# Kernel optimization log

Measured on AMD Instinct MI355X. Metric: run time of the kernel, lower is better.

## Reference

```python
import jax, jax.numpy as jnp
import numpy as np

PH = 12        # planning_horizon
B = 16         # batch
H = 256        # belief dim
Z = 64         # state dim
CAND = 512     # candidates
TOPK = 64      # top_candidates
ITERS = 3      # optimisation_iters
NTOOLS = 36    # num_tools
CONT = 2       # cont_action_size (hard-coded in source)
MIN_A, MAX_A = -1.0, 1.0


def setup_inputs() -> dict:
    ks = jax.random.split(jax.random.key(0), 9)
    s = 0.05  # weight scale keeps tanh in its linear-ish regime
    return {
        "belief": jax.random.normal(ks[0], (B, H), jnp.float32),
        "state": jax.random.normal(ks[1], (B, Z), jnp.float32),
        "Wb": jax.random.normal(ks[2], (H, H), jnp.float32) * s,
        "Wa": jax.random.normal(ks[3], (3, H), jnp.float32) * s,
        "bb": jnp.zeros((H,), jnp.float32),
        "Ws": jax.random.normal(ks[4], (H, Z), jnp.float32) * s,
        "bs": jnp.zeros((Z,), jnp.float32),
        "wrb": jax.random.normal(ks[5], (H,), jnp.float32) * s,
        "wrs": jax.random.normal(ks[6], (Z,), jnp.float32) * s,
    }


def reference(belief, state, Wb, Wa, bb, Ws, bs, wrb, wrs):
    # expand to (B*CAND, .) exactly like unsqueeze+expand+reshape (row-repeat)
    b0 = jnp.repeat(belief, CAND, axis=0)  # (B*CAND, H)
    s0 = jnp.repeat(state, CAND, axis=0)   # (B*CAND, Z)

    action_mean = jnp.zeros((PH, B, 1, CONT), jnp.float32)
    action_std = jnp.ones((PH, B, 1, CONT), jnp.float32)
    freq = jnp.ones((PH, B, 1, NTOOLS), jnp.float32)

    key = jax.random.key(42)
    for it in range(ITERS):
        k_disc, k_noise, key = jax.random.split(key, 3)
        # multinomial(freq, CAND, replacement=True) per (PH*B) row
        logits = jnp.log(freq.reshape(-1, NTOOLS))            # (PH*B, NTOOLS)
        disc = jax.random.categorical(k_disc, logits, shape=(CAND, PH * B)).T
        disc = disc.reshape(PH, B * CAND, 1).astype(jnp.float32)
        # continuous: mean + std * N(0,1), clamped
        noise = jax.random.normal(k_noise, (PH, B, CAND, CONT), jnp.float32)
        cont = jnp.clip(action_mean + action_std * noise, MIN_A, MAX_A)
        cont = cont.reshape(PH, B * CAND, CONT)
        actions = jnp.concatenate([disc, cont], axis=-1)       # (PH, B*CAND, 3)

        # rollout: stand-in recurrent transition + linear reward
        def step(carry, a_t):
            b, s_ = carry
            b = jnp.tanh(b @ Wb + a_t @ Wa + bb)
            s_ = jnp.tanh(b @ Ws + bs)
            return (b, s_), (b, s_)

        _, (beliefs, states) = jax.lax.scan(step, (b0, s0), actions)
        returns = (beliefs @ wrb + states @ wrs).sum(axis=0)   # (B*CAND,)

        # top-k candidates per batch element
        _, idx = jax.lax.top_k(returns.reshape(B, CAND), TOPK)  # (B, TOPK)
        actions_r = actions.reshape(PH, B, CAND, 1 + CONT)
        best = jnp.take_along_axis(actions_r, idx[None, :, :, None], axis=2)  # (PH,B,TOPK,3)

        cont_best = best[..., 1:]
        action_mean = cont_best.mean(axis=2, keepdims=True)
        action_std = jnp.std(cont_best, axis=2, keepdims=True)  # unbiased=False

        # batched histogram over TOPK discrete actions (histc with unit bins),
        # +1 smoothing, normalize -- one fused pass instead of PH*B histc calls
        dints = best[..., 0].astype(jnp.int32)                  # (PH, B, TOPK)
        hist = jax.nn.one_hot(dints, NTOOLS, dtype=jnp.float32).sum(axis=2) + 1.0
        freq = (hist / hist.sum(axis=-1, keepdims=True))[:, :, None, :]

    disc_final = jnp.argmax(freq[0, :, 0, :], axis=-1).astype(jnp.float32)[:, None]  # (B,1)
    cont_final = action_mean[0, :, 0, :]                                             # (B,CONT)
    return jnp.concatenate([disc_final, cont_final], axis=1)                         # (B,3)
```

## Files before the change

kernel.cpp:

```cpp
#include <hip/hip_runtime.h>
#include <cstdint>
#include <cmath>

#define PARTITIONABLE 1

constexpr int kPH = 12;
constexpr int kB = 16;
constexpr int kH = 256;
constexpr int kZ = 64;
constexpr int kCand = 512;
constexpr int kTopK = 64;
constexpr int kTools = 36;
constexpr int kRT = kB * kCand;
constexpr uint32_t kDiscTotal = (uint32_t)kCand * kPH * kB * kTools;
constexpr uint32_t kContTotal = (uint32_t)kPH * kB * kCand * 2;

constexpr int kRowsB = 16;
constexpr int kStrideB = 20;

__host__ __device__ inline void tf2x32(uint32_t k0, uint32_t k1,
                                       uint32_t x0, uint32_t x1,
                                       uint32_t& o0, uint32_t& o1) {
  uint32_t ks2 = k0 ^ k1 ^ 0x1BD11BDAu;
  x0 += k0; x1 += k1;
#define TFROT(v, d) (((v) << (d)) | ((v) >> (32 - (d))))
#define TFR(r) { x0 += x1; x1 = TFROT(x1, r); x1 ^= x0; }
  TFR(13) TFR(15) TFR(26) TFR(6)
  x0 += k1;  x1 += ks2 + 1u;
  TFR(17) TFR(29) TFR(16) TFR(24)
  x0 += ks2; x1 += k0 + 2u;
  TFR(13) TFR(15) TFR(26) TFR(6)
  x0 += k0;  x1 += k1 + 3u;
  TFR(17) TFR(29) TFR(16) TFR(24)
  x0 += k1;  x1 += ks2 + 4u;
  TFR(13) TFR(15) TFR(26) TFR(6)
  x0 += ks2; x1 += k0 + 5u;
#undef TFR
#undef TFROT
  o0 = x0; o1 = x1;
}

__device__ inline uint32_t jax_bits32(uint32_t k0, uint32_t k1,
                                      uint32_t idx, uint32_t total) {
#if PARTITIONABLE
  (void)total;
  uint32_t y0, y1;
  tf2x32(k0, k1, 0u, idx, y0, y1);
  return y0 ^ y1;
#else
  uint32_t half = total >> 1;
  uint32_t y0, y1;
  if (idx < half) { tf2x32(k0, k1, idx, idx + half, y0, y1); return y0; }
  else            { tf2x32(k0, k1, idx - half, idx, y0, y1); return y1; }
#endif
}

static void host_split3(uint32_t k0, uint32_t k1, uint32_t out[3][2]) {
#if PARTITIONABLE
  for (uint32_t i = 0; i < 3; ++i)
    tf2x32(k0, k1, 0u, i, out[i][0], out[i][1]);
#else
  uint32_t a0,a1,b0,b1,c0,c1;
  tf2x32(k0, k1, 0u, 3u, a0, a1);
  tf2x32(k0, k1, 1u, 4u, b0, b1);
  tf2x32(k0, k1, 2u, 5u, c0, c1);
  out[0][0]=a0; out[0][1]=b0;
  out[1][0]=c0; out[1][1]=a1;
  out[2][0]=b1; out[2][1]=c1;
#endif
}

__device__ inline float erfinv_xla(float x) {
  float xx = x * x;
  float w = -(float)log1p((double)(-xx));
  float p;
  if (w < 5.0f) {
    float ww = w - 2.5f;
    p = 2.81022636e-08f;
    p = fmaf(p, ww, 3.43273939e-07f);
    p = fmaf(p, ww, -3.5233877e-06f);
    p = fmaf(p, ww, -4.39150654e-06f);
    p = fmaf(p, ww, 0.00021858087f);
    p = fmaf(p, ww, -0.00125372503f);
    p = fmaf(p, ww, -0.00417768164f);
    p = fmaf(p, ww, 0.246640727f);
    p = fmaf(p, ww, 1.50140941f);
  } else {
    float ww = sqrtf(w) - 3.0f;
    p = -0.000200214257f;
    p = fmaf(p, ww, 0.000100950558f);
    p = fmaf(p, ww, 0.00134934322f);
    p = fmaf(p, ww, -0.00367342844f);
    p = fmaf(p, ww, 0.00573950773f);
    p = fmaf(p, ww, -0.0076224613f);
    p = fmaf(p, ww, 0.00943887047f);
    p = fmaf(p, ww, 1.00167406f);
    p = fmaf(p, ww, 2.83297682f);
  }
  return p * x;
}

__global__ __launch_bounds__(256) void k_sample_disc(
    uint32_t kd0, uint32_t kd1, const float* __restrict__ lfreq,
    float* __restrict__ discA, int it0) {
  int gid = blockIdx.x * 256 + threadIdx.x;
  if (gid >= kCand * kPH * kB) return;
  int c = gid / (kPH * kB);
  int j = gid - c * (kPH * kB);
  int best = 0;
  if (it0) {
    uint32_t bm = 0u;
    for (int t = 0; t < kTools; ++t) {
      uint32_t bits = jax_bits32(kd0, kd1, (uint32_t)(gid * kTools + t), kDiscTotal);
      uint32_t m = bits >> 9;
      if (t == 0 || m > bm) { bm = m; best = t; }
    }
  } else {
    const float* lf = lfreq + j * kTools;
    float bv = 0.0f;
    for (int t = 0; t < kTools; ++t) {
      uint32_t bits = jax_bits32(kd0, kd1, (uint32_t)(gid * kTools + t), kDiscTotal);
      float u = __uint_as_float((bits >> 9) | 0x3F800000u) - 1.0f;
      if (u == 0.0f) u = 1.17549435e-38f;
      float l1 = (float)log((double)u);
      float g = -(float)log((double)(-l1));
      float val = g + lf[t];
      if (t == 0 || val > bv) { bv = val; best = t; }
    }
  }
  int ph = j >> 4, b = j & 15;
  discA[ph * kRT + b * kCand + c] = (float)best;
}

__global__ __launch_bounds__(256) void k_sample_cont(
    uint32_t kn0, uint32_t kn1, const float* __restrict__ meanv,
    const float* __restrict__ stdv, float* __restrict__ contA, int it0) {
  int gid = blockIdx.x * 256 + threadIdx.x;
  if (gid >= (int)kContTotal) return;
  uint32_t bits = jax_bits32(kn0, kn1, (uint32_t)gid, kContTotal);
  float f = __uint_as_float((bits >> 9) | 0x3F800000u) - 1.0f;
  const float lo = -0.99999994f;
  float u = fmaxf(lo, f * 2.0f + lo);
  float n = __uint_as_float(0x3FB504F3u) * erfinv_xla(u);
  int d = gid & 1;
  int c = (gid >> 1) & (kCand - 1);
  int rest = gid >> 10;
  int ph = rest >> 4, b = rest & 15;
  float m, s;
  if (it0) { m = 0.0f; s = 1.0f; }
  else {
    m = meanv[rest * 2 + d];
    s = stdv[rest * 2 + d];
  }
  float x = m + s * n;
  x = fminf(fmaxf(x, -1.0f), 1.0f);
  contA[(ph * kRT + b * kCand + c) * 2 + d] = x;
}

__global__ __launch_bounds__(512, 4) void k_rollout(
    const float* __restrict__ belief,
    const float* __restrict__ discA, const float* __restrict__ contA,
    const float* __restrict__ Wb, const float* __restrict__ Wa,
    const float* __restrict__ bbv_, const float* __restrict__ Ws,
    const float* __restrict__ bs_, const float* __restrict__ wrb,
    const float* __restrict__ wrs, float* __restrict__ ret) {
  __shared__ float sBc[kH * kStrideB];
  __shared__ float pT[kRowsB * kH];
  __shared__ float sAD[kRowsB], sA0[kRowsB], sA1[kRowsB];
  __shared__ float sret[kRowsB];

  const int tid = threadIdx.x;
  const int row0 = blockIdx.x * kRowsB;
  const int batch = row0 >> 9;

  const int w = tid >> 6;
  const int kw = w >> 2;
  const int wc = w & 3;
  const int lane = tid & 63;
  const int lr = lane >> 5;
  const int lc = lane & 31;
  const int r0 = lr * 8;
  const int c0 = wc * 64 + lc * 2;
  const int kbase = kw * 128;

  const int lr2 = lane >> 4;
  const int lc2 = lane & 15;
  const int r0s = lr2 * 4;
  const int cs = wc * 16 + lc2;

  const float wa00 = Wa[c0],          wa01 = Wa[c0 + 1];
  const float wa10 = Wa[kH + c0],     wa11 = Wa[kH + c0 + 1];
  const float wa20 = Wa[2 * kH + c0], wa21 = Wa[2 * kH + c0 + 1];
  const float bb0 = bbv_[c0], bb1 = bbv_[c0 + 1];
  const float wrb0 = wrb[c0], wrb1 = wrb[c0 + 1];
  const float bsv = bs_[cs], wrsv = wrs[cs];

  for (int i = tid; i < kH * kRowsB; i += 512) {
    int k = i >> 4, r = i & (kRowsB - 1);
    sBc[k * kStrideB + r] = belief[batch * kH + k];
  }
  if (tid < kRowsB) sret[tid] = 0.0f;
  __syncthreads();

  #pragma unroll 1
  for (int ph = 0; ph < kPH; ++ph) {
    if (tid < kRowsB) {
      int gr = row0 + tid;
      sAD[tid] = discA[ph * kRT + gr];
      sA0[tid] = contA[(ph * kRT + gr) * 2 + 0];
      sA1[tid] = contA[(ph * kRT + gr) * 2 + 1];
    }
    __syncthreads();

    float acc[8][2];
    #pragma unroll
    for (int r = 0; r < 8; ++r) { acc[r][0] = 0.0f; acc[r][1] = 0.0f; }
    #pragma unroll 2
    for (int k = kbase; k < kbase + 128; ++k) {
      float4 a0 = *reinterpret_cast<const float4*>(&sBc[k * kStrideB + r0]);
      float4 a1 = *reinterpret_cast<const float4*>(&sBc[k * kStrideB + r0 + 4]);
      float2 w2 = *reinterpret_cast<const float2*>(&Wb[k * kH + c0]);
      float av[8] = {a0.x, a0.y, a0.z, a0.w, a1.x, a1.y, a1.z, a1.w};
      #pragma unroll
      for (int r = 0; r < 8; ++r) {
        acc[r][0] = fmaf(av[r], w2.x, acc[r][0]);
        acc[r][1] = fmaf(av[r], w2.y, acc[r][1]);
      }
    }
    if (kw == 1) {
      #pragma unroll
      for (int r = 0; r < 8; ++r) {
        pT[(r0 + r) * kH + c0]     = acc[r][0];
        pT[(r0 + r) * kH + c0 + 1] = acc[r][1];
      }
    }
    __syncthreads();

    if (kw == 0) {
      #pragma unroll
      for (int r = 0; r < 8; ++r) {
        int rb = r0 + r;
        float aD = sAD[rb], aC0 = sA0[rb], aC1 = sA1[rb];
        float t0 = acc[r][0] + pT[rb * kH + c0];
        float t1 = acc[r][1] + pT[rb * kH + c0 + 1];
        t0 += bb0 + aD * wa00 + aC0 * wa10 + aC1 * wa20;
        t1 += bb1 + aD * wa01 + aC0 * wa11 + aC1 * wa21;
        acc[r][0] = tanhf(t0);
        acc[r][1] = tanhf(t1);
      }
      float4 v;
      v = make_float4(acc[0][0], acc[1][0], acc[2][0], acc[3][0]);
      *reinterpret_cast<float4*>(&sBc[c0 * kStrideB + r0]) = v;
      v = make_float4(acc[4][0], acc[5][0], acc[6][0], acc[7][0]);
      *reinterpret_cast<float4*>(&sBc[c0 * kStrideB + r0 + 4]) = v;
      v = make_float4(acc[0][1], acc[1][1], acc[2][1], acc[3][1]);
      *reinterpret_cast<float4*>(&sBc[(c0 + 1) * kStrideB + r0]) = v;
      v = make_float4(acc[4][1], acc[5][1], acc[6][1], acc[7][1]);
      *reinterpret_cast<float4*>(&sBc[(c0 + 1) * kStrideB + r0 + 4]) = v;
    }
    __syncthreads();

    float sacc[4] = {0.0f, 0.0f, 0.0f, 0.0f};
    #pragma unroll 4
    for (int k = kbase; k < kbase + 128; ++k) {
      float4 a4 = *reinterpret_cast<const float4*>(&sBc[k * kStrideB + r0s]);
      float wv = Ws[k * kZ + cs];
      sacc[0] = fmaf(a4.x, wv, sacc[0]);
      sacc[1] = fmaf(a4.y, wv, sacc[1]);
      sacc[2] = fmaf(a4.z, wv, sacc[2]);
      sacc[3] = fmaf(a4.w, wv, sacc[3]);
    }
    if (kw == 1) {
      #pragma unroll
      for (int i = 0; i < 4; ++i) pT[(r0s + i) * kZ + cs] = sacc[i];
    }
    __syncthreads();

    if (kw == 0) {
      float rp[8];
      #pragma unroll
      for (int r = 0; r < 8; ++r)
        rp[r] = acc[r][0] * wrb0 + acc[r][1] * wrb1;
      #pragma unroll
      for (int sh = 1; sh < 32; sh <<= 1) {
        #pragma unroll
        for (int r = 0; r < 8; ++r) rp[r] += __shfl_xor(rp[r], sh, 64);
      }
      if (lc == 0) {
        #pragma unroll
        for (int r = 0; r < 8; ++r) atomicAdd(&sret[r0 + r], rp[r]);
      }
      float sp[4];
      #pragma unroll
      for (int i = 0; i < 4; ++i) {
        float sv = tanhf(sacc[i] + pT[(r0s + i) * kZ + cs] + bsv);
        sp[i] = sv * wrsv;
      }
      #pragma unroll
      for (int sh = 1; sh < 16; sh <<= 1) {
        #pragma unroll
        for (int i = 0; i < 4; ++i) sp[i] += __shfl_xor(sp[i], sh, 64);
      }
      if (lc2 == 0) {
        #pragma unroll
        for (int i = 0; i < 4; ++i) atomicAdd(&sret[r0s + i], sp[i]);
      }
    }
    __syncthreads();
  }
  if (tid < kRowsB) ret[row0 + tid] = sret[tid];
}

__global__ __launch_bounds__(256) void k_topk_stats(
    const float* __restrict__ ret, const float* __restrict__ discA,
    const float* __restrict__ contA, float* __restrict__ freq,
    float* __restrict__ lfreq, float* __restrict__ meanv,
    float* __restrict__ stdv) {
  __shared__ float rv[kCand];
  __shared__ int selc[kTopK];
  __shared__ int hist[kTools];
  const int b = blockIdx.x, tid = threadIdx.x;
  for (int i = tid; i < kCand; i += 256) rv[i] = ret[b * kCand + i];
  __syncthreads();
  for (int c = tid; c < kCand; c += 256) {
    float v = rv[c];
    int rank = 0;
    for (int o = 0; o < kCand; ++o) {
      float vo = rv[o];
      rank += ((vo > v) || (vo == v && o < c)) ? 1 : 0;
    }
    if (rank < kTopK) selc[rank] = c;
  }
  __syncthreads();
  for (int ph = 0; ph < kPH; ++ph) {
    if (tid < kTools) hist[tid] = 0;
    __syncthreads();
    if (tid < kTopK) {
      int c = selc[tid];
      int idx = ph * kRT + b * kCand + c;
      int d = (int)discA[idx];
      atomicAdd(&hist[d], 1);
      float c0 = contA[idx * 2 + 0];
      float c1 = contA[idx * 2 + 1];
      float s0 = c0, s1 = c1;
      #pragma unroll
      for (int sh = 1; sh < 64; sh <<= 1) {
        s0 += __shfl_xor(s0, sh, 64);
        s1 += __shfl_xor(s1, sh, 64);
      }
      float m0 = s0 * (1.0f / 64.0f);
      float m1 = s1 * (1.0f / 64.0f);
      float d0 = c0 - m0, d1 = c1 - m1;
      float q0 = d0 * d0, q1 = d1 * d1;
      #pragma unroll
      for (int sh = 1; sh < 64; sh <<= 1) {
        q0 += __shfl_xor(q0, sh, 64);
        q1 += __shfl_xor(q1, sh, 64);
      }
      if (tid == 0) {
        int o = (ph * kB + b) * 2;
        meanv[o + 0] = m0;
        meanv[o + 1] = m1;
        stdv[o + 0] = sqrtf(q0 * (1.0f / 64.0f));
        stdv[o + 1] = sqrtf(q1 * (1.0f / 64.0f));
      }
    }
    __syncthreads();
    if (tid < kTools) {
      float fq = (float)(hist[tid] + 1) / 100.0f;
      int o = (ph * kB + b) * kTools + tid;
      freq[o] = fq;
      lfreq[o] = (float)log((double)fq);
    }
    __syncthreads();
  }
}

__global__ void k_final(const float* __restrict__ freq,
                        const float* __restrict__ meanv,
                        float* __restrict__ out) {
  int b = threadIdx.x;
  if (b < kB) {
    const float* f = freq + b * kTools;
    int best = 0; float bv = f[0];
    for (int t = 1; t < kTools; ++t)
      if (f[t] > bv) { bv = f[t]; best = t; }
    out[b * 3 + 0] = (float)best;
    out[b * 3 + 1] = meanv[b * 2 + 0];
    out[b * 3 + 2] = meanv[b * 2 + 1];
  }
}

extern "C" void kernel_launch(void* const* d_in, const int* in_sizes, int n_in,
                              void* d_out, int out_size, void* d_ws, size_t ws_size,
                              hipStream_t stream) {
  (void)in_sizes; (void)n_in; (void)out_size; (void)ws_size;
  const float* belief = (const float*)d_in[0];
  const float* Wb  = (const float*)d_in[2];
  const float* Wa  = (const float*)d_in[3];
  const float* bb  = (const float*)d_in[4];
  const float* Ws  = (const float*)d_in[5];
  const float* bs  = (const float*)d_in[6];
  const float* wrb = (const float*)d_in[7];
  const float* wrs = (const float*)d_in[8];
  float* out = (float*)d_out;

  float* w = (float*)d_ws;
  float* discA = w;
  float* contA = discA + kPH * kRT;
  float* ret   = contA + kPH * kRT * 2;
  float* freq  = ret + kRT;
  float* lfreq = freq + kPH * kB * kTools;
  float* meanv = lfreq + kPH * kB * kTools;
  float* stdv  = meanv + kPH * kB * 2;

  uint32_t key0 = 0u, key1 = 42u;
  for (int it = 0; it < 3; ++it) {
    uint32_t ks[3][2];
    host_split3(key0, key1, ks);
    int it0 = (it == 0) ? 1 : 0;
    k_sample_disc<<<dim3((kCand * kPH * kB + 255) / 256), dim3(256), 0, stream>>>(
        ks[0][0], ks[0][1], lfreq, discA, it0);
    k_sample_cont<<<dim3((kContTotal + 255) / 256), dim3(256), 0, stream>>>(
        ks[1][0], ks[1][1], meanv, stdv, contA, it0);
    k_rollout<<<dim3(kRT / kRowsB), dim3(512), 0, stream>>>(
        belief, discA, contA, Wb, Wa, bb, Ws, bs, wrb, wrs, ret);
    k_topk_stats<<<dim3(kB), dim3(256), 0, stream>>>(
        ret, discA, contA, freq, lfreq, meanv, stdv);
    key0 = ks[2][0]; key1 = ks[2][1];
  }
  k_final<<<dim3(1), dim3(64), 0, stream>>>(freq, meanv, out);
}
```

Before: 1.198 ms.

## Retile rollout GEMM to 4x4 register blocks and defer reward reductions

```diff
diff --git a/kernel.cpp b/kernel.cpp
--- a/kernel.cpp
+++ b/kernel.cpp
@@ -166,7 +166,10 @@
     const float* __restrict__ wrs, float* __restrict__ ret) {
   __shared__ float sBc[kH * kStrideB];
   __shared__ float pT[kRowsB * kH];
-  __shared__ float sAD[kRowsB], sA0[kRowsB], sA1[kRowsB];
+  __shared__ float sPT[kRowsB * kZ];
+  __shared__ float sAD[kPH][kRowsB];
+  __shared__ float sA0[kPH][kRowsB];
+  __shared__ float sA1[kPH][kRowsB];
   __shared__ float sret[kRowsB];
 
   const int tid = threadIdx.x;
@@ -177,137 +180,141 @@
   const int kw = w >> 2;
   const int wc = w & 3;
   const int lane = tid & 63;
-  const int lr = lane >> 5;
-  const int lc = lane & 31;
-  const int r0 = lr * 8;
-  const int c0 = wc * 64 + lc * 2;
+  const int lr = lane >> 4;
+  const int lc = lane & 15;
+  const int r0 = lr * 4;
+  const int c0 = wc * 64 + lc * 4;
+  const int zc = wc * 16 + lc;
   const int kbase = kw * 128;
 
-  const int lr2 = lane >> 4;
-  const int lc2 = lane & 15;
-  const int r0s = lr2 * 4;
-  const int cs = wc * 16 + lc2;
-
-  const float wa00 = Wa[c0],          wa01 = Wa[c0 + 1];
-  const float wa10 = Wa[kH + c0],     wa11 = Wa[kH + c0 + 1];
-  const float wa20 = Wa[2 * kH + c0], wa21 = Wa[2 * kH + c0 + 1];
-  const float bb0 = bbv_[c0], bb1 = bbv_[c0 + 1];
-  const float wrb0 = wrb[c0], wrb1 = wrb[c0 + 1];
-  const float bsv = bs_[cs], wrsv = wrs[cs];
-
-  for (int i = tid; i < kH * kRowsB; i += 512) {
-    int k = i >> 4, r = i & (kRowsB - 1);
-    sBc[k * kStrideB + r] = belief[batch * kH + k];
+  const float4 bb4  = *reinterpret_cast<const float4*>(&bbv_[c0]);
+  const float4 wa04 = *reinterpret_cast<const float4*>(&Wa[c0]);
+  const float4 wa14 = *reinterpret_cast<const float4*>(&Wa[kH + c0]);
+  const float4 wa24 = *reinterpret_cast<const float4*>(&Wa[2 * kH + c0]);
+  const float4 wrb4 = *reinterpret_cast<const float4*>(&wrb[c0]);
+  const float bsv = bs_[zc], wrsv = wrs[zc];
+
+  if (tid < kH) {
+    float v = belief[batch * kH + tid];
+    #pragma unroll
+    for (int r = 0; r < kRowsB; ++r) sBc[tid * kStrideB + r] = v;
+  }
+  for (int i = tid; i < kPH * kRowsB; i += 512) {
+    int ph = i >> 4, r = i & 15;
+    int gr = row0 + r;
+    sAD[ph][r] = discA[ph * kRT + gr];
+    sA0[ph][r] = contA[(ph * kRT + gr) * 2 + 0];
+    sA1[ph][r] = contA[(ph * kRT + gr) * 2 + 1];
   }
   if (tid < kRowsB) sret[tid] = 0.0f;
+
+  float rsum[4] = {0.0f, 0.0f, 0.0f, 0.0f};
+  float ssum[4] = {0.0f, 0.0f, 0.0f, 0.0f};
   __syncthreads();
+
+  const float* bK = sBc + kbase * kStrideB + r0;
+  const float* wB = Wb + (size_t)kbase * kH + c0;
+  const float* wS = Ws + (size_t)kbase * kZ + zc;
 
   #pragma unroll 1
   for (int ph = 0; ph < kPH; ++ph) {
-    if (tid < kRowsB) {
-      int gr = row0 + tid;
-      sAD[tid] = discA[ph * kRT + gr];
-      sA0[tid] = contA[(ph * kRT + gr) * 2 + 0];
-      sA1[tid] = contA[(ph * kRT + gr) * 2 + 1];
-    }
-    __syncthreads();
-
-    float acc[8][2];
+    float acc[4][4];
     #pragma unroll
-    for (int r = 0; r < 8; ++r) { acc[r][0] = 0.0f; acc[r][1] = 0.0f; }
-    #pragma unroll 2
-    for (int k = kbase; k < kbase + 128; ++k) {
-      float4 a0 = *reinterpret_cast<const float4*>(&sBc[k * kStrideB + r0]);
-      float4 a1 = *reinterpret_cast<const float4*>(&sBc[k * kStrideB + r0 + 4]);
-      float2 w2 = *reinterpret_cast<const float2*>(&Wb[k * kH + c0]);
-      float av[8] = {a0.x, a0.y, a0.z, a0.w, a1.x, a1.y, a1.z, a1.w};
-      #pragma unroll
-      for (int r = 0; r < 8; ++r) {
-        acc[r][0] = fmaf(av[r], w2.x, acc[r][0]);
-        acc[r][1] = fmaf(av[r], w2.y, acc[r][1]);
-      }
+    for (int r = 0; r < 4; ++r)
+      #pragma unroll
+      for (int c = 0; c < 4; ++c) acc[r][c] = 0.0f;
+    #pragma unroll 4
+    for (int k = 0; k < 128; ++k) {
+      float4 bv = *reinterpret_cast<const float4*>(bK + k * kStrideB);
+      float4 wv = *reinterpret_cast<const float4*>(wB + k * kH);
+      acc[0][0] = fmaf(bv.x, wv.x, acc[0][0]);
+      acc[0][1] = fmaf(bv.x, wv.y, acc[0][1]);
+      acc[0][2] = fmaf(bv.x, wv.z, acc[0][2]);
+      acc[0][3] = fmaf(bv.x, wv.w, acc[0][3]);
+      acc[1][0] = fmaf(bv.y, wv.x, acc[1][0]);
+      acc[1][1] = fmaf(bv.y, wv.y, acc[1][1]);
+      acc[1][2] = fmaf(bv.y, wv.z, acc[1][2]);
+      acc[1][3] = fmaf(bv.y, wv.w, acc[1][3]);
+      acc[2][0] = fmaf(bv.z, wv.x, acc[2][0]);
+      acc[2][1] = fmaf(bv.z, wv.y, acc[2][1]);
+      acc[2][2] = fmaf(bv.z, wv.z, acc[2][2]);
+      acc[2][3] = fmaf(bv.z, wv.w, acc[2][3]);
+      acc[3][0] = fmaf(bv.w, wv.x, acc[3][0]);
+      acc[3][1] = fmaf(bv.w, wv.y, acc[3][1]);
+      acc[3][2] = fmaf(bv.w, wv.z, acc[3][2]);
+      acc[3][3] = fmaf(bv.w, wv.w, acc[3][3]);
     }
     if (kw == 1) {
       #pragma unroll
-      for (int r = 0; r < 8; ++r) {
-        pT[(r0 + r) * kH + c0]     = acc[r][0];
-        pT[(r0 + r) * kH + c0 + 1] = acc[r][1];
-      }
-    }
-    __syncthreads();
-
+      for (int r = 0; r < 4; ++r)
+        *reinterpret_cast<float4*>(&pT[(r0 + r) * kH + c0]) =
+            make_float4(acc[r][0], acc[r][1], acc[r][2], acc[r][3]);
+    }
+    __syncthreads();
     if (kw == 0) {
       #pragma unroll
-      for (int r = 0; r < 8; ++r) {
-        int rb = r0 + r;
-        float aD = sAD[rb], aC0 = sA0[rb], aC1 = sA1[rb];
-        float t0 = acc[r][0] + pT[rb * kH + c0];
-        float t1 = acc[r][1] + pT[rb * kH + c0 + 1];
-        t0 += bb0 + aD * wa00 + aC0 * wa10 + aC1 * wa20;
-        t1 += bb1 + aD * wa01 + aC0 * wa11 + aC1 * wa21;
+      for (int r = 0; r < 4; ++r) {
+        float4 p = *reinterpret_cast<const float4*>(&pT[(r0 + r) * kH + c0]);
+        float aD = sAD[ph][r0 + r], a0 = sA0[ph][r0 + r], a1 = sA1[ph][r0 + r];
+        float t0 = acc[r][0] + p.x + bb4.x + aD * wa04.x + a0 * wa14.x + a1 * wa24.x;
+        float t1 = acc[r][1] + p.y + bb4.y + aD * wa04.y + a0 * wa14.y + a1 * wa24.y;
+        float t2 = acc[r][2] + p.z + bb4.z + aD * wa04.z + a0 * wa14.z + a1 * wa24.z;
+        float t3 = acc[r][3] + p.w + bb4.w + aD * wa04.w + a0 * wa14.w + a1 * wa24.w;
         acc[r][0] = tanhf(t0);
         acc[r][1] = tanhf(t1);
-      }
-      float4 v;
-      v = make_float4(acc[0][0], acc[1][0], acc[2][0], acc[3][0]);
-      *reinterpret_cast<float4*>(&sBc[c0 * kStrideB + r0]) = v;
-      v = make_float4(acc[4][0], acc[5][0], acc[6][0], acc[7][0]);
-      *reinterpret_cast<float4*>(&sBc[c0 * kStrideB + r0 + 4]) = v;
-      v = make_float4(acc[0][1], acc[1][1], acc[2][1], acc[3][1]);
-      *reinterpret_cast<float4*>(&sBc[(c0 + 1) * kStrideB + r0]) = v;
-      v = make_float4(acc[4][1], acc[5][1], acc[6][1], acc[7][1]);
-      *reinterpret_cast<float4*>(&sBc[(c0 + 1) * kStrideB + r0 + 4]) = v;
-    }
-    __syncthreads();
-
-    float sacc[4] = {0.0f, 0.0f, 0.0f, 0.0f};
-    #pragma unroll 4
-    for (int k = kbase; k < kbase + 128; ++k) {
-      float4 a4 = *reinterpret_cast<const float4*>(&sBc[k * kStrideB + r0s]);
-      float wv = Ws[k * kZ + cs];
-      sacc[0] = fmaf(a4.x, wv, sacc[0]);
-      sacc[1] = fmaf(a4.y, wv, sacc[1]);
-      sacc[2] = fmaf(a4.z, wv, sacc[2]);
-      sacc[3] = fmaf(a4.w, wv, sacc[3]);
+        acc[r][2] = tanhf(t2);
+        acc[r][3] = tanhf(t3);
+      }
+      #pragma unroll
+      for (int c = 0; c < 4; ++c)
+        *reinterpret_cast<float4*>(&sBc[(c0 + c) * kStrideB + r0]) =
+            make_float4(acc[0][c], acc[1][c], acc[2][c], acc[3][c]);
+      #pragma unroll
+      for (int r = 0; r < 4; ++r) {
+        rsum[r] = fmaf(acc[r][0], wrb4.x, rsum[r]);
+        rsum[r] = fmaf(acc[r][1], wrb4.y, rsum[r]);
+        rsum[r] = fmaf(acc[r][2], wrb4.z, rsum[r]);
+        rsum[r] = fmaf(acc[r][3], wrb4.w, rsum[r]);
+      }
+    }
+    __syncthreads();
+
+    float sa[4] = {0.0f, 0.0f, 0.0f, 0.0f};
+    #pragma unroll 8
+    for (int k = 0; k < 128; ++k) {
+      float4 bv = *reinterpret_cast<const float4*>(bK + k * kStrideB);
+      float wv = wS[k * kZ];
+      sa[0] = fmaf(bv.x, wv, sa[0]);
+      sa[1] = fmaf(bv.y, wv, sa[1]);
+      sa[2] = fmaf(bv.z, wv, sa[2]);
+      sa[3] = fmaf(bv.w, wv, sa[3]);
     }
     if (kw == 1) {
       #pragma unroll
-      for (int i = 0; i < 4; ++i) pT[(r0s + i) * kZ + cs] = sacc[i];
-    }
-    __syncthreads();
-
+      for (int r = 0; r < 4; ++r) sPT[(r0 + r) * kZ + zc] = sa[r];
+    }
+    __syncthreads();
     if (kw == 0) {
-      float rp[8];
-      #pragma unroll
-      for (int r = 0; r < 8; ++r)
-        rp[r] = acc[r][0] * wrb0 + acc[r][1] * wrb1;
-      #pragma unroll
-      for (int sh = 1; sh < 32; sh <<= 1) {
-        #pragma unroll
-        for (int r = 0; r < 8; ++r) rp[r] += __shfl_xor(rp[r], sh, 64);
-      }
-      if (lc == 0) {
-        #pragma unroll
-        for (int r = 0; r < 8; ++r) atomicAdd(&sret[r0 + r], rp[r]);
-      }
-      float sp[4];
-      #pragma unroll
-      for (int i = 0; i < 4; ++i) {
-        float sv = tanhf(sacc[i] + pT[(r0s + i) * kZ + cs] + bsv);
-        sp[i] = sv * wrsv;
-      }
-      #pragma unroll
-      for (int sh = 1; sh < 16; sh <<= 1) {
-        #pragma unroll
-        for (int i = 0; i < 4; ++i) sp[i] += __shfl_xor(sp[i], sh, 64);
-      }
-      if (lc2 == 0) {
-        #pragma unroll
-        for (int i = 0; i < 4; ++i) atomicAdd(&sret[r0s + i], sp[i]);
-      }
-    }
-    __syncthreads();
-  }
+      #pragma unroll
+      for (int r = 0; r < 4; ++r) {
+        float sv = tanhf(sa[r] + sPT[(r0 + r) * kZ + zc] + bsv);
+        ssum[r] = fmaf(sv, wrsv, ssum[r]);
+      }
+    }
+  }
+
+  if (kw == 0) {
+    #pragma unroll
+    for (int r = 0; r < 4; ++r) {
+      float v = rsum[r] + ssum[r];
+      v += __shfl_xor(v, 1, 64);
+      v += __shfl_xor(v, 2, 64);
+      v += __shfl_xor(v, 4, 64);
+      v += __shfl_xor(v, 8, 64);
+      if (lc == 0) atomicAdd(&sret[r0 + r], v);
+    }
+  }
+  __syncthreads();
   if (tid < kRowsB) ret[row0 + tid] = sret[tid];
 }
 
```

Measured after the change: 1.083 ms. -9.7%, faster.
